# Kernel optimization log

Measured on AMD Instinct MI355X. Metric: run time of the kernel, lower is better.

The kernel has to match this reference:

```python
import jax, jax.numpy as jnp
import numpy as np

N_TOKENS = 4096
EMBED = 2048
D_ATTN = 2048


def setup_inputs() -> dict:
    key = jax.random.key(0)
    k1, k2, k3, k4 = jax.random.split(key, 4)
    # torch.rand -> uniform [0,1); keeps scores positive so the multiplicative
    # -inf mask acts as a clean causal mask (faithful to original behavior).
    token_embeddings = jax.random.uniform(k1, (N_TOKENS, EMBED), dtype=jnp.float32)
    W_Q = jax.random.uniform(k2, (EMBED, D_ATTN), dtype=jnp.float32)
    W_K = jax.random.uniform(k3, (EMBED, D_ATTN), dtype=jnp.float32)
    W_V = jax.random.uniform(k4, (EMBED, D_ATTN), dtype=jnp.float32)
    return {"token_embeddings": token_embeddings, "W_Q": W_Q, "W_K": W_K, "W_V": W_V}


def reference(token_embeddings, W_Q, W_K, W_V):
    n = token_embeddings.shape[0]
    d = W_Q.shape[1]
    # mask: 1 on/below diagonal, -inf strictly above (multiplicative, as in source)
    neg_inf = jnp.float32(-jnp.inf)
    mask = jnp.tril(jnp.ones((n, n), dtype=jnp.float32)) + jnp.triu(
        jnp.full((n, n), neg_inf, dtype=jnp.float32), k=1
    )
    Q = token_embeddings @ W_Q          # (n, d)
    K = token_embeddings @ W_K          # (n, d)
    V = token_embeddings @ W_V          # (n, d)
    scores = (Q @ K.T) * mask           # (n, n); upper tri -> -inf (scores > 0)
    scores = scores / jnp.sqrt(jnp.float32(d))
    attn = jax.nn.softmax(scores, axis=-1)
    return attn @ V                     # (n, d)
```

## Files before the change

kernel.cpp:

```cpp
#include <hip/hip_runtime.h>
#include <hip/hip_bf16.h>
#include <cstdint>
#include <cstddef>
#include <cmath>

#define N_TOK 4096
#define EMB   2048
#define DATT  2048

typedef __attribute__((ext_vector_type(8))) short short8;
typedef __attribute__((ext_vector_type(4))) short shortx4;
typedef __attribute__((ext_vector_type(4))) float f32x4;

#define MFMA(a, b, c) __builtin_amdgcn_mfma_f32_16x16x32_bf16(a, b, c, 0, 0, 0)

__device__ __forceinline__ short f2bs(float f) {
  __hip_bfloat16 h = __float2bfloat16(f);
  return __builtin_bit_cast(short, h);
}
__device__ __forceinline__ float bs2f(short s) {
  return __uint_as_float(((unsigned)(unsigned short)s) << 16);
}
__device__ __forceinline__ float ldin(const void* p, size_t i, int isbf) {
  if (isbf) {
    unsigned short u = ((const unsigned short*)p)[i];
    return __uint_as_float(((unsigned int)u) << 16);
  }
  return ((const float*)p)[i];
}

__device__ __forceinline__ size_t swz(int r, int c, int kdim) {
  return ((size_t)((r >> 7) * (kdim >> 3) + (c >> 3)) << 10) +
         (size_t)((r & 127) << 3) + (c & 7);
}

__device__ __forceinline__ void gl16(const short* g, short* l) {
  __builtin_amdgcn_global_load_lds(
      (const __attribute__((address_space(1))) unsigned int*)(const void*)g,
      (__attribute__((address_space(3))) unsigned int*)(void*)l, 16, 0, 0);
}

template <bool THREE>
__device__ __forceinline__ void gemm_core(const short* Ah, const short* Al,
                                          const short* Bh, const short* Bl,
                                          int chunks, int apan, int bpan,
                                          int kmax, short* lds,
                                          f32x4 acc[4][4]) {
  const int NSL = THREE ? 4 : 2;
  int tid = threadIdx.x;
  int lane = tid & 63;
  int wave = tid >> 6;
  int ln = lane & 15, quad = lane >> 4;
  int wm = (wave >> 1) * 64, wn = (wave & 1) * 64;
  int wofs = wave * 512;

  auto stage = [&](int b, int k0) {
    size_t ao = ((size_t)(apan * chunks + (k0 >> 3))) << 10;
    size_t bo = ((size_t)(bpan * chunks + (k0 >> 3))) << 10;
    short* base = lds + b * NSL * 4096;
    const short* sa = Ah + ao + tid * 8;
    const short* sb = Bh + bo + tid * 8;
    gl16(sa,        base + wofs);
    gl16(sa + 2048, base + wofs + 2048);
    gl16(sb,        base + 4096 + wofs);
    gl16(sb + 2048, base + 4096 + wofs + 2048);
    if (THREE) {
      const short* sal = Al + ao + tid * 8;
      const short* sbl = Bl + bo + tid * 8;
      gl16(sal,        base + 8192 + wofs);
      gl16(sal + 2048, base + 8192 + wofs + 2048);
      gl16(sbl,        base + 12288 + wofs);
      gl16(sbl + 2048, base + 12288 + wofs + 2048);
    }
  };

  stage(0, 0);
  int cur = 0;
  int abase = quad * 1024 + (wm + ln) * 8;
  int bbase = quad * 1024 + (wn + ln) * 8;
  for (int k0 = 0; k0 < kmax; k0 += 32) {
    __syncthreads();
    if (k0 + 32 < kmax) stage(cur ^ 1, k0 + 32);
    const short* B0 = lds + cur * NSL * 4096;
    short8 fah[4], fbh[4];
#pragma unroll
    for (int i = 0; i < 4; ++i) fah[i] = *(const short8*)(B0 + abase + i * 128);
#pragma unroll
    for (int j = 0; j < 4; ++j) fbh[j] = *(const short8*)(B0 + 4096 + bbase + j * 128);
    if (THREE) {
      short8 fal[4], fbl[4];
#pragma unroll
      for (int i = 0; i < 4; ++i) fal[i] = *(const short8*)(B0 + 8192 + abase + i * 128);
#pragma unroll
      for (int j = 0; j < 4; ++j) fbl[j] = *(const short8*)(B0 + 12288 + bbase + j * 128);
#pragma unroll
      for (int j = 0; j < 4; ++j)
#pragma unroll
        for (int i = 0; i < 4; ++i) {
          acc[i][j] = MFMA(fah[i], fbh[j], acc[i][j]);
          acc[i][j] = MFMA(fah[i], fbl[j], acc[i][j]);
          acc[i][j] = MFMA(fal[i], fbh[j], acc[i][j]);
        }
    } else {
#pragma unroll
      for (int j = 0; j < 4; ++j)
#pragma unroll
        for (int i = 0; i < 4; ++i) acc[i][j] = MFMA(fah[i], fbh[j], acc[i][j]);
    }
    cur ^= 1;
  }
}

__device__ __forceinline__ void gemm1d2(const short* __restrict__ Ah,
                                        const short* __restrict__ Bh,
                                        int chunks, int apan, int bpan,
                                        int kmax, short* lds, f32x4 acc[4][4]) {
  int tid = threadIdx.x;
  int lane = tid & 63, wave = tid >> 6;
  int ln = lane & 15, quad = lane >> 4;
  int wm = (wave >> 1) * 64, wn = (wave & 1) * 64;
  int wofs = wave * 512;
  int nt = kmax >> 5;

  auto stage = [&](int b, int t) {
    size_t ao = ((size_t)(apan * chunks + (t << 2))) << 10;
    size_t bo = ((size_t)(bpan * chunks + (t << 2))) << 10;
    short* base = lds + b * 8192;
    gl16(Ah + ao + tid * 8,        base + wofs);
    gl16(Ah + ao + 2048 + tid * 8, base + wofs + 2048);
    gl16(Bh + bo + tid * 8,        base + 4096 + wofs);
    gl16(Bh + bo + 2048 + tid * 8, base + 4096 + wofs + 2048);
  };
  stage(0, 0);
  if (nt > 1) stage(1, 1);

  int abase = quad * 1024 + (wm + ln) * 8;
  int bbase = quad * 1024 + (wn + ln) * 8;
  int bi = 0;
  for (int t = 0; t < nt; ++t) {
    if (t + 1 < nt) asm volatile("s_waitcnt vmcnt(4)" ::: "memory");
    else            asm volatile("s_waitcnt vmcnt(0)" ::: "memory");
    __builtin_amdgcn_s_barrier();
    __builtin_amdgcn_sched_barrier(0);
    int pi = bi + 2; if (pi > 2) pi -= 3;
    if (t + 2 < nt) stage(pi, t + 2);
    const short* L = lds + bi * 8192;
    short8 fah[4], fbh[4];
#pragma unroll
    for (int i = 0; i < 4; ++i) fah[i] = *(const short8*)(L + abase + i * 128);
#pragma unroll
    for (int j = 0; j < 4; ++j) fbh[j] = *(const short8*)(L + 4096 + bbase + j * 128);
#pragma unroll
    for (int j = 0; j < 4; ++j)
#pragma unroll
      for (int i = 0; i < 4; ++i) acc[i][j] = MFMA(fah[i], fbh[j], acc[i][j]);
    ++bi; if (bi > 2) bi = 0;
  }
}

__global__ void k_sniff(const void* x, int* flag) {
  if (threadIdx.x == 0 && blockIdx.x == 0) {
    const unsigned short* u = (const unsigned short*)x;
    int bf = 1;
    for (int i = 0; i < 256; ++i) {
      unsigned short v = u[i];
      if ((v & 0x8000u) || ((v & 0x7FFFu) >= 0x3F80u)) { bf = 0; break; }
    }
    *flag = bf;
  }
}

__global__ __launch_bounds__(256) void k_xbar(const void* X, float* xbar,
                                              const int* flagp) {
  int isbf = *flagp;
  int e = blockIdx.x * 256 + threadIdx.x;
  float s = 0.f;
  for (int r = 0; r < 256; ++r) s += ldin(X, (size_t)r * EMB + e, isbf);
  xbar[e] = s * (1.f / 256.f);
}

__global__ __launch_bounds__(256) void k_split_x(const void* X, short* Xh, short* Xl,
                                                 const int* flagp) {
  int isbf = *flagp;
  size_t base = ((size_t)blockIdx.x * 256 + threadIdx.x) * 4;
  int r = (int)(base >> 11), c = (int)(base & 2047);
  shortx4 h, l;
#pragma unroll
  for (int u = 0; u < 4; ++u) {
    float x = ldin(X, base + u, isbf);
    short hh = f2bs(x);
    h[u] = hh;
    l[u] = f2bs(x - bs2f(hh));
  }
  size_t o = swz(r, c, EMB);
  *(shortx4*)(Xh + o) = h;
  *(shortx4*)(Xl + o) = l;
}

__global__ __launch_bounds__(256) void k_transpose_split(const void* W, short* Wth,
                                                         short* Wtl, int R, int C,
                                                         const int* flagp, int wlo) {
  __shared__ float T[64][65];
  int isbf = *flagp;
  int r0 = blockIdx.y * 64, c0 = blockIdx.x * 64;
  int tid = threadIdx.x;
#pragma unroll
  for (int it = 0; it < 16; ++it) {
    int idx = tid + it * 256;
    int row = idx >> 6, col = idx & 63;
    T[row][col] = ldin(W, (size_t)(r0 + row) * C + c0 + col, isbf);
  }
  __syncthreads();
#pragma unroll
  for (int it = 0; it < 16; ++it) {
    int idx = tid + it * 256;
    int row = idx >> 6, col = idx & 63;
    float x = T[col][row];
    short h = f2bs(x);
    size_t o = swz(c0 + row, r0 + col, R);
    Wth[o] = h;
    if (wlo) Wtl[o] = f2bs(x - bs2f(h));
  }
}

__global__ __launch_bounds__(256) void k_kbar(const short* Wth, const short* Wtl,
                                              const float* xbar, float* kbar) {
  int d = blockIdx.x;
  float s = 0.f;
  for (int e = threadIdx.x; e < EMB; e += 256) {
    size_t o = swz(d, e, EMB);
    s += xbar[e] * (bs2f(Wth[o]) + bs2f(Wtl[o]));
  }
  __shared__ float red[4];
#pragma unroll
  for (int off = 32; off > 0; off >>= 1) s += __shfl_down(s, off);
  if ((threadIdx.x & 63) == 0) red[threadIdx.x >> 6] = s;
  __syncthreads();
  if (threadIdx.x == 0) kbar[d] = red[0] + red[1] + red[2] + red[3];
}

__global__ __launch_bounds__(256, 2) void k_proj3(const short* Ah, const short* Al,
                                                  const short* Bh, const short* Bl,
                                                  short* Ch, short* Cl,
                                                  const float* bias) {
  __shared__ short lds[2 * 16384];
  int bid = blockIdx.x;
  int s = ((bid & 7) << 6) | (bid >> 3);
  int row0 = (s >> 4) << 7, col0 = (s & 15) << 7;
  f32x4 acc[4][4] = {};
  gemm_core<true>(Ah, Al, Bh, Bl, EMB >> 3, row0 >> 7, col0 >> 7, EMB, lds, acc);
  int tid = threadIdx.x;
  int wave = tid >> 6, lane = tid & 63;
  int ln = lane & 15, quad = lane >> 4;
  int wm = (wave >> 1) * 64, wn = (wave & 1) * 64;
#pragma unroll
  for (int i = 0; i < 4; ++i)
#pragma unroll
    for (int j = 0; j < 4; ++j)
#pragma unroll
      for (int r = 0; r < 4; ++r) {
        int row = row0 + wm + i * 16 + quad * 4 + r;
        int col = col0 + wn + j * 16 + ln;
        float x = acc[i][j][r];
        if (bias) x -= bias[col];
        short h = f2bs(x);
        size_t o = swz(row, col, DATT);
        Ch[o] = h;
        Cl[o] = f2bs(x - bs2f(h));
      }
}

__global__ __launch_bounds__(256, 3) void k_proj1(const short* Ah, const short* Bh,
                                                  short* Ch) {
  __shared__ short lds[3 * 8192];
  int bid = blockIdx.x;
  int s = ((bid & 7) << 6) | (bid >> 3);
  int row0 = (s >> 5) << 7, col0 = (s & 31) << 7;
  f32x4 acc[4][4] = {};
  gemm1d2(Ah, Bh, EMB >> 3, row0 >> 7, col0 >> 7, EMB, lds, acc);
  int tid = threadIdx.x;
  int wave = tid >> 6, lane = tid & 63;
  int ln = lane & 15, quad = lane >> 4;
  int wm = (wave >> 1) * 64, wn = (wave & 1) * 64;
#pragma unroll
  for (int i = 0; i < 4; ++i)
#pragma unroll
    for (int j = 0; j < 4; ++j)
#pragma unroll
      for (int r = 0; r < 4; ++r) {
        int row = row0 + wm + i * 16 + quad * 4 + r;
        int col = col0 + wn + j * 16 + ln;
        Ch[swz(row, col, N_TOK)] = f2bs(acc[i][j][r]);
      }
}

__global__ __launch_bounds__(256, 2) void k_score3(const short* Qh, const short* Ql,
                                                   const short* Kh, const short* Kl,
                                                   float* S) {
  int bi0 = blockIdx.x;
  int bi = (bi0 & 7) * 66 + (bi0 >> 3);
  int by = (int)((sqrtf(8.f * (float)bi + 1.f) - 1.f) * 0.5f);
  while ((by + 1) * (by + 2) / 2 <= bi) ++by;
  while (by * (by + 1) / 2 > bi) --by;
  int bx = bi - by * (by + 1) / 2;
  __shared__ short lds[2 * 16384];
  f32x4 acc[4][4] = {};
  gemm_core<true>(Qh, Ql, Kh, Kl, DATT >> 3, by, bx, DATT, lds, acc);
  int row0 = by * 128, col0 = bx * 128;
  int tid = threadIdx.x;
  int wave = tid >> 6, lane = tid & 63;
  int ln = lane & 15, quad = lane >> 4;
  int wm = (wave >> 1) * 64, wn = (wave & 1) * 64;
  const float scale = 0.022097086912079608f;
#pragma unroll
  for (int i = 0; i < 4; ++i)
#pragma unroll
    for (int j = 0; j < 4; ++j)
#pragma unroll
      for (int r = 0; r < 4; ++r) {
        int row = row0 + wm + i * 16 + quad * 4 + r;
        int col = col0 + wn + j * 16 + ln;
        if (col <= row) S[(size_t)row * N_TOK + col] = acc[i][j][r] * scale;
      }
}

__global__ __launch_bounds__(256) void k_softmax(const float* S, short* P) {
  int i = blockIdx.x;
  const float* row = S + (size_t)i * N_TOK;
  int len = i + 1;
  int tid = threadIdx.x;
  __shared__ float red[4];
  float m = -3.402823466e38f;
  for (int j = tid; j < len; j += 256) m = fmaxf(m, row[j]);
#pragma unroll
  for (int off = 32; off > 0; off >>= 1) m = fmaxf(m, __shfl_down(m, off));
  if ((tid & 63) == 0) red[tid >> 6] = m;
  __syncthreads();
  m = fmaxf(fmaxf(red[0], red[1]), fmaxf(red[2], red[3]));
  __syncthreads();
  float s = 0.f;
  for (int j = tid; j < len; j += 256) s += __expf(row[j] - m);
#pragma unroll
  for (int off = 32; off > 0; off >>= 1) s += __shfl_down(s, off);
  if ((tid & 63) == 0) red[tid >> 6] = s;
  __syncthreads();
  s = red[0] + red[1] + red[2] + red[3];
  float inv = 1.f / s;
  size_t rbase = ((size_t)(i >> 7) * (N_TOK >> 3) << 10) + (size_t)((i & 127) << 3);
  for (int j = tid; j < len; j += 256)
    P[rbase + ((size_t)(j >> 3) << 10) + (j & 7)] = f2bs(__expf(row[j] - m) * inv);
  for (int j = len + tid; j < N_TOK; j += 256)
    P[rbase + ((size_t)(j >> 3) << 10) + (j & 7)] = 0;
}

__global__ __launch_bounds__(256, 3) void k_out(const short* Ph, const short* Vh,
                                                void* Co, const int* flagp) {
  __shared__ short lds[3 * 8192];
  int bid = blockIdx.x;
  int half = bid >> 8;
  int r = bid & 255;
  int s = ((r & 7) << 5) | (r >> 3);
  int bb = s >> 4;
  int band = half ? bb : (31 - bb);
  int row0 = band << 7, col0 = (s & 15) << 7;
  f32x4 acc[4][4] = {};
  gemm1d2(Ph, Vh, N_TOK >> 3, row0 >> 7, col0 >> 7, row0 + 128, lds, acc);
  int isbf = *flagp;
  int tid = threadIdx.x;
  int wave = tid >> 6, lane = tid & 63;
  int ln = lane & 15, quad = lane >> 4;
  int wm = (wave >> 1) * 64, wn = (wave & 1) * 64;
#pragma unroll
  for (int i = 0; i < 4; ++i)
#pragma unroll
    for (int j = 0; j < 4; ++j)
#pragma unroll
      for (int r2 = 0; r2 < 4; ++r2) {
        int row = row0 + wm + i * 16 + quad * 4 + r2;
        int col = col0 + wn + j * 16 + ln;
        size_t idx = (size_t)row * DATT + col;
        if (isbf) ((__hip_bfloat16*)Co)[idx] = __float2bfloat16(acc[i][j][r2]);
        else      ((float*)Co)[idx] = acc[i][j][r2];
      }
}

extern "C" void kernel_launch(void* const* d_in, const int* in_sizes, int n_in,
                              void* d_out, int out_size, void* d_ws, size_t ws_size,
                              hipStream_t stream) {
  const void* X  = d_in[0];
  const void* WQ = d_in[1];
  const void* WK = d_in[2];
  const void* WV = d_in[3];

  float* ws   = (float*)d_ws;
  int*   flag = (int*)d_ws;
  float* xbar = ws + 256;
  float* kbar = ws + 2560;
  short* p0   = (short*)(ws + 16384);
  const size_t M8 = (size_t)N_TOK * DATT;
  const size_t M4 = (size_t)EMB * DATT;
  short* Xh  = p0;
  short* Xl  = Xh + M8;
  short* Wth = Xl + M8;
  short* Wtl = Wth + M4;
  float* S   = (float*)p0;
  short* Qh  = p0 + 4 * M8;
  short* Ql  = Qh + M8;
  short* Kh  = Ql + M8;
  short* Kl  = Kh + M8;
  short* Vt  = Kl + M8;
  short* P   = Qh;

  dim3 blk(256);

  k_sniff<<<1, 64, 0, stream>>>(X, flag);
  k_xbar<<<EMB / 256, blk, 0, stream>>>(X, xbar, flag);
  k_split_x<<<(N_TOK * EMB) / 1024, blk, 0, stream>>>(X, Xh, Xl, flag);

  dim3 gt(DATT / 64, EMB / 64);

  k_transpose_split<<<gt, blk, 0, stream>>>(WQ, Wth, Wtl, EMB, DATT, flag, 1);
  k_proj3<<<dim3(512), blk, 0, stream>>>(Xh, Xl, Wth, Wtl, Qh, Ql, nullptr);
  k_transpose_split<<<gt, blk, 0, stream>>>(WK, Wth, Wtl, EMB, DATT, flag, 1);
  k_kbar<<<DATT, blk, 0, stream>>>(Wth, Wtl, xbar, kbar);
  k_proj3<<<dim3(512), blk, 0, stream>>>(Xh, Xl, Wth, Wtl, Kh, Kl, kbar);
  k_transpose_split<<<gt, blk, 0, stream>>>(WV, Wth, nullptr, EMB, DATT, flag, 0);
  k_proj1<<<dim3(512), blk, 0, stream>>>(Wth, Xh, Vt);

  k_score3<<<dim3(528), blk, 0, stream>>>(Qh, Ql, Kh, Kl, S);

  k_softmax<<<N_TOK, blk, 0, stream>>>(S, P);

  k_out<<<dim3(512), blk, 0, stream>>>(P, Vt, d_out, flag);
}
```

Measured before the change: 660.0 us.

## Use 256x128 tiles with 8 waves and triple-buffered pipeline for Q/K projections

The split-precision Q and K projection GEMMs move from 128x128 tiles with 4 waves and double buffering to 256x128 tiles with 512-thread blocks. The new loop uses three LDS buffers, prefetches two steps ahead with interleaved loads, and raises wave priority around the MFMAs. The larger tile reuses each loaded B panel across more rows and hides load latency better, at the cost of 144 KB of LDS per block, which may limit occupancy to one block per CU. Separately, softmax now zero-fills P only up to the next 128-column boundary instead of the full row, since the output GEMM only reads up to the causal limit.

```diff
diff --git a/kernel.cpp b/kernel.cpp
--- a/kernel.cpp
+++ b/kernel.cpp
@@ -111,6 +111,86 @@
   }
 }
 
+template <int AP, int BP>
+__device__ __forceinline__ void gemm8(const short* __restrict__ Ah,
+                                      const short* __restrict__ Al,
+                                      const short* __restrict__ Bh,
+                                      const short* __restrict__ Bl,
+                                      int chunks, int apan, int bpan,
+                                      int kmax, short* lds, f32x4 acc[4][4]) {
+  constexpr int ASZ = AP * 4096;
+  constexpr int BSZ = BP * 4096;
+  constexpr int OAL = ASZ;
+  constexpr int OBH = 2 * ASZ;
+  constexpr int OBL = 2 * ASZ + BSZ;
+  constexpr int BUF = 2 * ASZ + 2 * BSZ;
+  constexpr int NNW = BP * 2;
+  int tid = threadIdx.x;
+  int lane = tid & 63, wave = tid >> 6;
+  int ln = lane & 15, quad = lane >> 4;
+  int wm = (wave / NNW) * 64, wn = (wave % NNW) * 64;
+  int nt = kmax >> 5;
+
+  auto sp = [&](int b, int t, int p) {
+    short* base = lds + b * BUF;
+    const short* g;
+    short* l;
+    if (p < AP)               { g = Ah + (((size_t)(apan + p) * chunks + (t << 2)) << 10);          l = base + p * 4096; }
+    else if (p < 2 * AP)      { int q = p - AP;      g = Al + (((size_t)(apan + q) * chunks + (t << 2)) << 10); l = base + OAL + q * 4096; }
+    else if (p < 2 * AP + BP) { int q = p - 2 * AP;  g = Bh + (((size_t)(bpan + q) * chunks + (t << 2)) << 10); l = base + OBH + q * 4096; }
+    else                      { int q = p - 2 * AP - BP; g = Bl + (((size_t)(bpan + q) * chunks + (t << 2)) << 10); l = base + OBL + q * 4096; }
+    gl16(g + tid * 8, l + wave * 512);
+  };
+
+#pragma unroll
+  for (int p = 0; p < 6; ++p) sp(0, 0, p);
+  if (nt > 1) {
+#pragma unroll
+    for (int p = 0; p < 6; ++p) sp(1, 1, p);
+  }
+
+  int abase = (wm & 128) * 32 + quad * 1024 + ((wm & 64) + ln) * 8;
+  int bbase = (wn & 128) * 32 + quad * 1024 + ((wn & 64) + ln) * 8;
+  int bi = 0;
+  for (int t = 0; t < nt; ++t) {
+    if (t + 1 < nt) asm volatile("s_waitcnt vmcnt(6)" ::: "memory");
+    else            asm volatile("s_waitcnt vmcnt(0)" ::: "memory");
+    __builtin_amdgcn_s_barrier();
+    __builtin_amdgcn_sched_barrier(0);
+
+    const short* L = lds + bi * BUF;
+    int pi = bi + 2; if (pi > 2) pi -= 3;
+    bool pf = (t + 2 < nt);
+
+    short8 bh[4], bl[4];
+#pragma unroll
+    for (int j = 0; j < 4; ++j) {
+      bh[j] = *(const short8*)(L + OBH + bbase + j * 128);
+      bl[j] = *(const short8*)(L + OBL + bbase + j * 128);
+    }
+#pragma unroll
+    for (int i = 0; i < 4; ++i) {
+      short8 ah = *(const short8*)(L + abase + i * 128);
+      short8 al = *(const short8*)(L + OAL + abase + i * 128);
+      if (pf) {
+        if (i == 0)      { sp(pi, t + 2, 0); sp(pi, t + 2, 1); }
+        else if (i == 1) { sp(pi, t + 2, 2); sp(pi, t + 2, 3); }
+        else if (i == 2) { sp(pi, t + 2, 4); }
+        else             { sp(pi, t + 2, 5); }
+      }
+      __builtin_amdgcn_s_setprio(1);
+#pragma unroll
+      for (int j = 0; j < 4; ++j) {
+        acc[i][j] = MFMA(ah, bh[j], acc[i][j]);
+        acc[i][j] = MFMA(ah, bl[j], acc[i][j]);
+        acc[i][j] = MFMA(al, bh[j], acc[i][j]);
+      }
+      __builtin_amdgcn_s_setprio(0);
+    }
+    ++bi; if (bi > 2) bi = 0;
+  }
+}
+
 __device__ __forceinline__ void gemm1d2(const short* __restrict__ Ah,
                                         const short* __restrict__ Bh,
                                         int chunks, int apan, int bpan,
@@ -239,16 +319,16 @@
   if (threadIdx.x == 0) kbar[d] = red[0] + red[1] + red[2] + red[3];
 }
 
-__global__ __launch_bounds__(256, 2) void k_proj3(const short* Ah, const short* Al,
+__global__ __launch_bounds__(512, 2) void k_proj3(const short* Ah, const short* Al,
                                                   const short* Bh, const short* Bl,
                                                   short* Ch, short* Cl,
                                                   const float* bias) {
-  __shared__ short lds[2 * 16384];
+  __shared__ short lds[3 * 24576];
   int bid = blockIdx.x;
-  int s = ((bid & 7) << 6) | (bid >> 3);
-  int row0 = (s >> 4) << 7, col0 = (s & 15) << 7;
+  int s = ((bid & 7) << 5) | (bid >> 3);
+  int row0 = (s >> 4) << 8, col0 = (s & 15) << 7;
   f32x4 acc[4][4] = {};
-  gemm_core<true>(Ah, Al, Bh, Bl, EMB >> 3, row0 >> 7, col0 >> 7, EMB, lds, acc);
+  gemm8<2, 1>(Ah, Al, Bh, Bl, EMB >> 3, row0 >> 7, col0 >> 7, EMB, lds, acc);
   int tid = threadIdx.x;
   int wave = tid >> 6, lane = tid & 63;
   int ln = lane & 15, quad = lane >> 4;
@@ -349,7 +429,8 @@
   size_t rbase = ((size_t)(i >> 7) * (N_TOK >> 3) << 10) + (size_t)((i & 127) << 3);
   for (int j = tid; j < len; j += 256)
     P[rbase + ((size_t)(j >> 3) << 10) + (j & 7)] = f2bs(__expf(row[j] - m) * inv);
-  for (int j = len + tid; j < N_TOK; j += 256)
+  int fillend = (len + 127) & ~127;
+  for (int j = len + tid; j < fillend; j += 256)
     P[rbase + ((size_t)(j >> 3) << 10) + (j & 7)] = 0;
 }
 
@@ -412,6 +493,7 @@
   short* P   = Qh;
 
   dim3 blk(256);
+  dim3 blk512(512);
 
   k_sniff<<<1, 64, 0, stream>>>(X, flag);
   k_xbar<<<EMB / 256, blk, 0, stream>>>(X, xbar, flag);
@@ -420,10 +502,10 @@
   dim3 gt(DATT / 64, EMB / 64);
 
   k_transpose_split<<<gt, blk, 0, stream>>>(WQ, Wth, Wtl, EMB, DATT, flag, 1);
-  k_proj3<<<dim3(512), blk, 0, stream>>>(Xh, Xl, Wth, Wtl, Qh, Ql, nullptr);
+  k_proj3<<<dim3(256), blk512, 0, stream>>>(Xh, Xl, Wth, Wtl, Qh, Ql, nullptr);
   k_transpose_split<<<gt, blk, 0, stream>>>(WK, Wth, Wtl, EMB, DATT, flag, 1);
   k_kbar<<<DATT, blk, 0, stream>>>(Wth, Wtl, xbar, kbar);
-  k_proj3<<<dim3(512), blk, 0, stream>>>(Xh, Xl, Wth, Wtl, Kh, Kl, kbar);
+  k_proj3<<<dim3(256), blk512, 0, stream>>>(Xh, Xl, Wth, Wtl, Kh, Kl, kbar);
   k_transpose_split<<<gt, blk, 0, stream>>>(WV, Wth, nullptr, EMB, DATT, flag, 0);
   k_proj1<<<dim3(512), blk, 0, stream>>>(Wth, Xh, Vt);
 
```

Measured after the change: 630.6 us. 1.05x faster.
